# Kernel tuning notes

Hardware: AMD Instinct MI355X
Metric: run time of the kernel (lower is better)

## Reference

```python
import jax, jax.numpy as jnp
import numpy as np

B, T, D, H = 4, 2048, 1024, 16
HD = D // H

def setup_inputs() -> dict:
    key = jax.random.key(0)
    ks = jax.random.split(key, 12)
    s = 0.02
    return {
        "query": jax.random.normal(ks[0], (B, T, D), dtype=jnp.float32),
        "key_": jax.random.normal(ks[1], (B, T, D), dtype=jnp.float32),
        "value": jax.random.normal(ks[2], (B, T, D), dtype=jnp.float32),
        "attention_mask": jnp.zeros((B, T, T), dtype=bool),
        "Wq": jax.random.normal(ks[3], (D, D), dtype=jnp.float32) * s,
        "bq": jnp.zeros((D,), dtype=jnp.float32),
        "Wk": jax.random.normal(ks[4], (D, D), dtype=jnp.float32) * s,
        "bk": jnp.zeros((D,), dtype=jnp.float32),
        "Wv": jax.random.normal(ks[5], (D, D), dtype=jnp.float32) * s,
        "bv": jnp.zeros((D,), dtype=jnp.float32),
        "Wo": jax.random.normal(ks[6], (D, D), dtype=jnp.float32) * s,
        "bo": jnp.zeros((D,), dtype=jnp.float32),
    }

def reference(query, key_, value, attention_mask, Wq, bq, Wk, bk, Wv, bv, Wo, bo):
    scale = 1.0 / jnp.sqrt(jnp.float32(HD))
    # projections (torch Linear: x @ W.T + b), split heads -> [B, H, T, HD]
    q = (query @ Wq.T + bq).reshape(B, T, H, HD).transpose(0, 2, 1, 3)
    k = (key_ @ Wk.T + bk).reshape(B, T, H, HD).transpose(0, 2, 1, 3)
    v = (value @ Wv.T + bv).reshape(B, T, H, HD).transpose(0, 2, 1, 3)
    scores = jnp.einsum('bhqd,bhkd->bhqk', q, k) * scale  # [B,H,T,T]
    mask = attention_mask[:, None, :, :]  # [B,1,T,T], True = masked
    scores = jnp.where(mask, -jnp.inf, scores)
    attn = jax.nn.softmax(scores, axis=-1)
    out = jnp.einsum('bhqk,bhkd->bhqd', attn, v)  # [B,H,T,HD]
    out = out.transpose(0, 2, 1, 3).reshape(B, T, D)
    return out @ Wo.T + bo
```

## Files before the change

### kernel.cpp

```cpp
#include <hip/hip_runtime.h>
#include <hip/hip_bf16.h>
#include <math.h>


typedef short bf16x8 __attribute__((ext_vector_type(8)));
typedef short bf16x4 __attribute__((ext_vector_type(4)));
typedef float f32x4  __attribute__((ext_vector_type(4)));
typedef float f32x16 __attribute__((ext_vector_type(16)));
typedef unsigned u32x4v __attribute__((ext_vector_type(4)));

#define DEV __device__ __forceinline__

DEV short f2bf(float f) {
    union { float f; unsigned u; } x; x.f = f;
    unsigned r = x.u + 0x7fffu + ((x.u >> 16) & 1u);
    return (short)(r >> 16);
}

DEV unsigned cvtpk(float lo, float hi) {
    unsigned r;
    asm("v_cvt_pk_bf16_f32 %0, %1, %2" : "=v"(r) : "v"(lo), "v"(hi));
    return r;
}

DEV void pl32swap(unsigned &a, unsigned &b) {
    asm volatile("v_permlane32_swap_b32 %0, %1" : "+v"(a), "+v"(b));
}

DEV float fexp2(float x) {
    float r;
    asm("v_exp_f32 %0, %1\n\ts_nop 0" : "=v"(r) : "v"(x));
    return r;
}

DEV void gload16(const void* g, void* lds_wave_base) {
    __builtin_amdgcn_global_load_lds(
        (const __attribute__((address_space(1))) void*)g,
        (__attribute__((address_space(3))) void*)lds_wave_base, 16, 0, 0);
}

DEV f32x4 mfma16(bf16x8 a, bf16x8 b, f32x4 c) {
    return __builtin_amdgcn_mfma_f32_16x16x32_bf16(a, b, c, 0, 0, 0);
}
DEV f32x16 mfma32(bf16x8 a, bf16x8 b, f32x16 c) {
    return __builtin_amdgcn_mfma_f32_32x32x16_bf16(a, b, c, 0, 0, 0);
}

__global__ __launch_bounds__(256) void cvt_one(const float* __restrict__ in,
                                               short* __restrict__ out) {
    int i = (blockIdx.x * 256 + threadIdx.x) * 8;
    f32x4 a = *(const f32x4*)(in + i);
    f32x4 b = *(const f32x4*)(in + i + 4);
    bf16x8 v;
    v[0]=f2bf(a[0]); v[1]=f2bf(a[1]); v[2]=f2bf(a[2]); v[3]=f2bf(a[3]);
    v[4]=f2bf(b[0]); v[5]=f2bf(b[1]); v[6]=f2bf(b[2]); v[7]=f2bf(b[3]);
    *(bf16x8*)(out + i) = v;
}

__global__ __launch_bounds__(256) void cvt_w4(
    const float* __restrict__ a, const float* __restrict__ b,
    const float* __restrict__ c, const float* __restrict__ d,
    short* __restrict__ oa, short* __restrict__ ob,
    short* __restrict__ oc, short* __restrict__ od) {
    const int sel = blockIdx.x >> 9;
    const float* in = sel == 0 ? a : sel == 1 ? b : sel == 2 ? c : d;
    short* out      = sel == 0 ? oa : sel == 1 ? ob : sel == 2 ? oc : od;
    int i = ((blockIdx.x & 511) * 256 + threadIdx.x) * 8;
    f32x4 x = *(const f32x4*)(in + i);
    f32x4 y = *(const f32x4*)(in + i + 4);
    bf16x8 v;
    v[0]=f2bf(x[0]); v[1]=f2bf(x[1]); v[2]=f2bf(x[2]); v[3]=f2bf(x[3]);
    v[4]=f2bf(y[0]); v[5]=f2bf(y[1]); v[6]=f2bf(y[2]); v[7]=f2bf(y[3]);
    *(bf16x8*)(out + i) = v;
}

template<int EPI>
__global__ __launch_bounds__(256) void gemm_bt(
    const short* __restrict__ A, const short* __restrict__ W,
    const float* __restrict__ bias, void* __restrict__ Cp, float epiScale)
{
    __shared__ short Alds[2][4096];
    __shared__ short Blds[2][4096];

    const int t = threadIdx.x;
    const int wave = t >> 6, lane = t & 63;
    const int lr = lane & 15, lg = lane >> 4;
    const int wg = (blockIdx.x & 7) * 64 + (blockIdx.x >> 3);
    const int m0 = (wg >> 3) * 128, n0 = (wg & 7) * 128;
    const int wr = wave >> 1, wc = wave & 1;

    const int o0 = t * 16,        kb0 = o0 >> 11, row0 = (o0 >> 4) & 127;
    const int o1 = 4096 + t * 16, kb1 = o1 >> 11, row1 = (o1 >> 4) & 127;
    const short* As0 = A + (size_t)(m0 + row0) * 1024 + kb0 * 8;
    const short* As1 = A + (size_t)(m0 + row1) * 1024 + kb1 * 8;
    const short* Ws0 = W + (size_t)(n0 + row0) * 1024 + kb0 * 8;
    const short* Ws1 = W + (size_t)(n0 + row1) * 1024 + kb1 * 8;

    auto stage = [&](short* dA, short* dB, int k0) {
        gload16(As0 + k0, (char*)dA + wave * 1024);
        gload16(As1 + k0, (char*)dA + 4096 + wave * 1024);
        gload16(Ws0 + k0, (char*)dB + wave * 1024);
        gload16(Ws1 + k0, (char*)dB + 4096 + wave * 1024);
    };

    f32x4 acc[4][4] = {};

    stage(Alds[0], Blds[0], 0);

    auto kstep = [&](int ts, int BUF) {
        if (ts < 31) {
            stage(Alds[BUF ^ 1], Blds[BUF ^ 1], (ts + 1) * 32);
            asm volatile("s_waitcnt vmcnt(4)" ::: "memory");
        } else {
            asm volatile("s_waitcnt vmcnt(0)" ::: "memory");
        }
        __builtin_amdgcn_s_barrier();
        bf16x8 af[4], bfr[4];
        #pragma unroll
        for (int mi = 0; mi < 4; mi++)
            af[mi] = *(const bf16x8*)(Alds[BUF] + lg * 1024 + (wr * 64 + mi * 16 + lr) * 8);
        #pragma unroll
        for (int ni = 0; ni < 4; ni++)
            bfr[ni] = *(const bf16x8*)(Blds[BUF] + lg * 1024 + (wc * 64 + ni * 16 + lr) * 8);
        #pragma unroll
        for (int mi = 0; mi < 4; mi++)
            #pragma unroll
            for (int ni = 0; ni < 4; ni++)
                acc[mi][ni] = mfma16(af[mi], bfr[ni], acc[mi][ni]);
        __builtin_amdgcn_s_barrier();
    };

    #pragma unroll 1
    for (int it = 0; it < 16; ++it) { kstep(2 * it, 0); kstep(2 * it + 1, 1); }

    #pragma unroll
    for (int mi = 0; mi < 4; mi++) {
        #pragma unroll
        for (int ni = 0; ni < 4; ni++) {
            const int n      = n0 + wc * 64 + ni * 16 + lr;
            const int m_base = m0 + wr * 64 + mi * 16 + lg * 4;
            const float bv   = bias[n];
            f32x4 a = acc[mi][ni];
            if constexpr (EPI == 0) {
                short* C = (short*)Cp;
                #pragma unroll
                for (int r = 0; r < 4; r++)
                    C[(size_t)(m_base + r) * 1024 + n] = f2bf((a[r] + bv) * epiScale);
            } else if constexpr (EPI == 2) {
                short* C = (short*)Cp;
                const int b = m_base >> 11, tt = m_base & 2047;
                bf16x4 p;
                #pragma unroll
                for (int r = 0; r < 4; r++) p[r] = f2bf(a[r] + bv);
                *(bf16x4*)(C + (size_t)b * 2097152 + (size_t)n * 2048 + tt) = p;
            } else {
                float* C = (float*)Cp;
                #pragma unroll
                for (int r = 0; r < 4; r++)
                    C[(size_t)(m_base + r) * 1024 + n] = a[r] + bv;
            }
        }
    }
}

__global__ __launch_bounds__(256) void mask_scan(const unsigned char* __restrict__ mask,
                                                 unsigned char* __restrict__ flags) {
    __shared__ int anyk[32];
    const int t = threadIdx.x, kt = t & 31, g = t >> 5;
    const int b = blockIdx.x >> 6, qt = blockIdx.x & 63;
    if (t < 32) anyk[t] = 0;
    __syncthreads();
    unsigned acc = 0;
    const unsigned char* base = mask + ((size_t)b * 2048 + qt * 32 + g * 4) * 2048 + kt * 64;
    #pragma unroll
    for (int rr = 0; rr < 4; rr++) {
        const uint4* p = (const uint4*)(base + (size_t)rr * 2048);
        #pragma unroll
        for (int s = 0; s < 4; s++) { uint4 v = p[s]; acc |= v.x | v.y | v.z | v.w; }
    }
    if (acc) anyk[kt] = 1;
    __syncthreads();
    if (t < 32) flags[((size_t)b * 64 + qt) * 32 + t] = (unsigned char)anyk[t];
}

__global__ __launch_bounds__(256, 2) void attn_fwd2(
    const short* __restrict__ Q, const short* __restrict__ K,
    const short* __restrict__ Vt, const unsigned char* __restrict__ mask,
    const unsigned char* __restrict__ flags, short* __restrict__ O)
{
    __shared__ short lds[2][2][4096];

    const int t = threadIdx.x, wave = t >> 6, lane = t & 63;
    const int j31 = lane & 31, hi = lane >> 5;

    const int raw = blockIdx.x;
    const int wg  = (raw & 7) * 128 + (raw >> 3);
    const int qblk = wg & 15, bh = wg >> 4;
    const int h = bh & 15, b = bh >> 4;
    const int q0 = qblk * 128 + wave * 32;

    bf16x8 qf[4];
    {
        const short* qp = Q + ((size_t)b * 2048 + q0 + j31) * 1024 + h * 64 + hi * 8;
        #pragma unroll
        for (int ck = 0; ck < 4; ck++) qf[ck] = *(const bf16x8*)(qp + ck * 16);
    }
    unsigned long long fmask;
    {
        unsigned char fb = flags[((size_t)b * 64 + qblk * 4 + wave) * 32 + j31];
        fmask = __ballot(fb != 0);
    }

    const short* Kg = K + ((size_t)b * 2048) * 1024 + h * 64;
    const short* Vg = Vt + (size_t)b * 2097152 + (size_t)h * 64 * 2048;

    auto stage = [&](short* dK, short* dV, int tk) {
        #pragma unroll
        for (int i = 0; i < 2; i++) {
            const int slot = i * 256 + t, row = slot >> 3;
            const int cs = ((slot & 7) ^ (row & 7)) * 8;
            gload16(Kg + (size_t)(tk + row) * 1024 + cs, dK + i * 2048 + wave * 512);
            gload16(Vg + (size_t)row * 2048 + tk + cs, dV + i * 2048 + wave * 512);
        }
    };

    stage(&lds[0][0][0], &lds[0][1][0], 0);

    f32x16 oA = {}, oB = {};
    float m = -1e30f, l = 0.f;
    const int sw = j31 & 7;

    auto tile = [&](int J, int BUF) {
        if (J < 31) {
            stage(&lds[BUF ^ 1][0][0], &lds[BUF ^ 1][1][0], (J + 1) * 64);
            asm volatile("s_waitcnt vmcnt(4)" ::: "memory");
        } else {
            asm volatile("s_waitcnt vmcnt(0)" ::: "memory");
        }
        __builtin_amdgcn_s_barrier();
        const short* ldsK = &lds[BUF][0][0];
        const short* ldsV = &lds[BUF][1][0];

        f32x16 sA = {}, sB = {};
        __builtin_amdgcn_s_setprio(1);
        #pragma unroll
        for (int ck = 0; ck < 4; ck++) {
            bf16x8 kf0 = *(const bf16x8*)(ldsK + j31 * 64        + (((2*ck + hi) ^ sw) * 8));
            bf16x8 kf1 = *(const bf16x8*)(ldsK + (32 + j31) * 64 + (((2*ck + hi) ^ sw) * 8));
            sA = mfma32(kf0, qf[ck], sA);
            sB = mfma32(kf1, qf[ck], sB);
        }
        __builtin_amdgcn_s_setprio(0);

        if ((fmask >> J) & 1ULL) {
            const unsigned char* mp = mask + ((size_t)b * 2048 + q0 + j31) * 2048
                                           + (size_t)J * 64 + hi * 4;
            #pragma unroll
            for (int a2 = 0; a2 < 2; a2++)
                #pragma unroll
                for (int rg = 0; rg < 4; rg++) {
                    unsigned mb = *(const unsigned*)(mp + a2 * 32 + rg * 8);
                    #pragma unroll
                    for (int e = 0; e < 4; e++) {
                        if ((mb >> (8 * e)) & 0xFFu) {
                            if (a2 == 0) sA[rg * 4 + e] = -1e30f;
                            else         sB[rg * 4 + e] = -1e30f;
                        }
                    }
                }
        }

        float tm = fmaxf(sA[0], sA[1]);
        #pragma unroll
        for (int r = 2; r < 16; r += 2) tm = fmaxf(fmaxf(tm, sA[r]), sA[r + 1]);
        #pragma unroll
        for (int r = 0; r < 16; r += 2) tm = fmaxf(fmaxf(tm, sB[r]), sB[r + 1]);
        tm = fmaxf(tm, __shfl_xor(tm, 32));
        if (!__all(tm <= m + 8.f)) {
            const float mnew = fmaxf(m, tm);
            const float fs = fexp2(m - mnew);
            m = mnew; l *= fs;
            #pragma unroll
            for (int r = 0; r < 16; r++) { oA[r] *= fs; oB[r] *= fs; }
        }
        float ps = 0.f;
        #pragma unroll
        for (int r = 0; r < 16; r++) { sA[r] = fexp2(sA[r] - m); ps += sA[r]; }
        #pragma unroll
        for (int r = 0; r < 16; r++) { sB[r] = fexp2(sB[r] - m); ps += sB[r]; }
        ps += __shfl_xor(ps, 32);
        l += ps;

        bf16x8 pb[4];
        #pragma unroll
        for (int c = 0; c < 4; c++) {
            const int rb = 8 * (c & 1);
            unsigned A0, B0, A1, B1;
            if (c < 2) {
                A0 = cvtpk(sA[rb],     sA[rb + 1]); B0 = cvtpk(sA[rb + 4], sA[rb + 5]);
                A1 = cvtpk(sA[rb + 2], sA[rb + 3]); B1 = cvtpk(sA[rb + 6], sA[rb + 7]);
            } else {
                A0 = cvtpk(sB[rb],     sB[rb + 1]); B0 = cvtpk(sB[rb + 4], sB[rb + 5]);
                A1 = cvtpk(sB[rb + 2], sB[rb + 3]); B1 = cvtpk(sB[rb + 6], sB[rb + 7]);
            }
            pl32swap(A0, B0); pl32swap(A1, B1);
            union { unsigned u[4]; bf16x8 v; } pu;
            pu.u[0] = A0; pu.u[1] = A1; pu.u[2] = B0; pu.u[3] = B1;
            pb[c] = pu.v;
        }

        __builtin_amdgcn_s_setprio(1);
        #pragma unroll
        for (int c = 0; c < 4; c++) {
            bf16x8 vf0 = *(const bf16x8*)(ldsV + j31 * 64        + (((2*c + hi) ^ sw) * 8));
            bf16x8 vf1 = *(const bf16x8*)(ldsV + (32 + j31) * 64 + (((2*c + hi) ^ sw) * 8));
            oA = mfma32(vf0, pb[c], oA);
            oB = mfma32(vf1, pb[c], oB);
        }
        __builtin_amdgcn_s_setprio(0);
        __builtin_amdgcn_s_barrier();
    };

    #pragma unroll 1
    for (int jj = 0; jj < 16; ++jj) { tile(2 * jj, 0); tile(2 * jj + 1, 1); }

    __syncthreads();
    unsigned* ow = (unsigned*)&lds[0][0][0] + wave * (32 * 34);
    const float inv = 1.f / l;
    #pragma unroll
    for (int o = 0; o < 2; o++)
        #pragma unroll
        for (int rp = 0; rp < 8; rp++) {
            const int r  = 2 * rp;
            const int hd = 2 * (rp & 1) + 8 * (rp >> 1) + 4 * hi + 32 * o;
            const float v0 = (o ? oB[r]     : oA[r])     * inv;
            const float v1 = (o ? oB[r + 1] : oA[r + 1]) * inv;
            ow[j31 * 34 + (hd >> 1)] = cvtpk(v0, v1);
        }
    __syncthreads();
    {
        const size_t orow = ((size_t)b * 2048 + q0 + j31) * 1024 + h * 64 + hi * 32;
        unsigned* gout = (unsigned*)(O + orow);
        const unsigned* src = ow + j31 * 34 + hi * 16;
        #pragma unroll
        for (int i = 0; i < 4; i++) {
            u32x4v v;
            v[0] = src[i*4]; v[1] = src[i*4+1]; v[2] = src[i*4+2]; v[3] = src[i*4+3];
            *(u32x4v*)(gout + i * 4) = v;
        }
    }
}

extern "C" void kernel_launch(void* const* d_in, const int* in_sizes, int n_in,
                              void* d_out, int out_size, void* d_ws, size_t ws_size,
                              hipStream_t stream)
{
    const float* query = (const float*)d_in[0];
    const float* key_  = (const float*)d_in[1];
    const float* value = (const float*)d_in[2];
    const unsigned char* amask = (const unsigned char*)d_in[3];
    const float* Wq = (const float*)d_in[4];
    const float* bq = (const float*)d_in[5];
    const float* Wk = (const float*)d_in[6];
    const float* bk = (const float*)d_in[7];
    const float* Wv = (const float*)d_in[8];
    const float* bv = (const float*)d_in[9];
    const float* Wo = (const float*)d_in[10];
    const float* bo = (const float*)d_in[11];
    float* out = (float*)d_out;

    char* ws = (char*)d_ws;
    const size_t MB = 1024 * 1024;
    short* Wqb = (short*)(ws + 0 * MB);
    short* Wkb = (short*)(ws + 2 * MB);
    short* Wvb = (short*)(ws + 4 * MB);
    short* Wob = (short*)(ws + 6 * MB);
    short* Qb  = (short*)(ws + 8 * MB);
    short* Kb  = (short*)(ws + 24 * MB);
    short* Vtb = (short*)(ws + 40 * MB);
    short* Xb  = (short*)(ws + 56 * MB);
    unsigned char* flagsb = (unsigned char*)(ws + 0 * MB);

    cvt_w4<<<2048, 256, 0, stream>>>(Wq, Wk, Wv, Wo, Wqb, Wkb, Wvb, Wob);

    const float qscale = 0.125f * 1.44269504088896f;
    cvt_one<<<4096, 256, 0, stream>>>(query, Xb);
    gemm_bt<0><<<512, 256, 0, stream>>>(Xb, Wqb, bq, Qb, qscale);
    cvt_one<<<4096, 256, 0, stream>>>(key_, Xb);
    gemm_bt<0><<<512, 256, 0, stream>>>(Xb, Wkb, bk, Kb, 1.0f);
    cvt_one<<<4096, 256, 0, stream>>>(value, Xb);
    gemm_bt<2><<<512, 256, 0, stream>>>(Xb, Wvb, bv, Vtb, 1.0f);

    mask_scan<<<256, 256, 0, stream>>>(amask, flagsb);

    attn_fwd2<<<1024, 256, 0, stream>>>(Qb, Kb, Vtb, amask, flagsb, Xb);

    gemm_bt<3><<<512, 256, 0, stream>>>(Xb, Wob, bo, out, 1.0f);
}
```

Measured before the change: 286.1 us.

## Fuse fp32 input conversion into batched QKV GEMM and widen attention KV tiles

Drops the three separate activation-conversion kernels and the three projection GEMM launches. A single gemm_qkv kernel now loads fp32 activations into registers, converts them to bf16 into LDS, and prefetches the next k-step. The attention kernel processes 128-key tiles instead of 64, using a larger LDS buffer and a wider V swizzle. It also computes the softmax row sum with an extra MFMA against a ones vector rather than scalar adds plus a shuffle. The weight conversion switches to packed cvt instructions. The aim is to cut launches and intermediate bf16 traffic and to halve the attention barrier count, at the cost of more register pressure and LDS use per block.

```diff
diff --git a/kernel.cpp b/kernel.cpp
--- a/kernel.cpp
+++ b/kernel.cpp
@@ -44,17 +44,6 @@
 }
 DEV f32x16 mfma32(bf16x8 a, bf16x8 b, f32x16 c) {
     return __builtin_amdgcn_mfma_f32_32x32x16_bf16(a, b, c, 0, 0, 0);
-}
-
-__global__ __launch_bounds__(256) void cvt_one(const float* __restrict__ in,
-                                               short* __restrict__ out) {
-    int i = (blockIdx.x * 256 + threadIdx.x) * 8;
-    f32x4 a = *(const f32x4*)(in + i);
-    f32x4 b = *(const f32x4*)(in + i + 4);
-    bf16x8 v;
-    v[0]=f2bf(a[0]); v[1]=f2bf(a[1]); v[2]=f2bf(a[2]); v[3]=f2bf(a[3]);
-    v[4]=f2bf(b[0]); v[5]=f2bf(b[1]); v[6]=f2bf(b[2]); v[7]=f2bf(b[3]);
-    *(bf16x8*)(out + i) = v;
 }
 
 __global__ __launch_bounds__(256) void cvt_w4(
@@ -68,16 +57,124 @@
     int i = ((blockIdx.x & 511) * 256 + threadIdx.x) * 8;
     f32x4 x = *(const f32x4*)(in + i);
     f32x4 y = *(const f32x4*)(in + i + 4);
-    bf16x8 v;
-    v[0]=f2bf(x[0]); v[1]=f2bf(x[1]); v[2]=f2bf(x[2]); v[3]=f2bf(x[3]);
-    v[4]=f2bf(y[0]); v[5]=f2bf(y[1]); v[6]=f2bf(y[2]); v[7]=f2bf(y[3]);
-    *(bf16x8*)(out + i) = v;
-}
-
-template<int EPI>
-__global__ __launch_bounds__(256) void gemm_bt(
+    union { unsigned u[4]; bf16x8 v; } p;
+    p.u[0] = cvtpk(x[0], x[1]); p.u[1] = cvtpk(x[2], x[3]);
+    p.u[2] = cvtpk(y[0], y[1]); p.u[3] = cvtpk(y[2], y[3]);
+    *(bf16x8*)(out + i) = p.v;
+}
+
+__global__ __launch_bounds__(256) void gemm_qkv(
+    const float* __restrict__ Aq, const float* __restrict__ Ak, const float* __restrict__ Av,
+    const short* __restrict__ Wqb, const short* __restrict__ Wkb, const short* __restrict__ Wvb,
+    const float* __restrict__ bqp, const float* __restrict__ bkp, const float* __restrict__ bvp,
+    short* __restrict__ Qo, short* __restrict__ Ko, short* __restrict__ Vo, float qscale)
+{
+    __shared__ short Alds[2][4096];
+    __shared__ short Blds[2][4096];
+
+    const int t = threadIdx.x, wave = t >> 6, lane = t & 63;
+    const int lr = lane & 15, lg = lane >> 4;
+    const int raw = blockIdx.x;
+    const int wg = (raw & 7) * 192 + (raw >> 3);
+    const int sel = wg >> 9, inner = wg & 511;
+    const int m0 = (inner >> 3) * 128, n0 = (inner & 7) * 128;
+    const int wr = wave >> 1, wc = wave & 1;
+
+    const float* A    = sel == 0 ? Aq  : sel == 1 ? Ak  : Av;
+    const short* W    = sel == 0 ? Wqb : sel == 1 ? Wkb : Wvb;
+    const float* bias = sel == 0 ? bqp : sel == 1 ? bkp : bvp;
+
+    const int arow = t & 127, kh = t >> 7;
+    const float* Asrc = A + (size_t)(m0 + arow) * 1024 + kh * 16;
+    const int o0 = t * 16,        kb0 = o0 >> 11, row0 = (o0 >> 4) & 127;
+    const int o1 = 4096 + t * 16, kb1 = o1 >> 11, row1 = (o1 >> 4) & 127;
+    const short* Ws0 = W + (size_t)(n0 + row0) * 1024 + kb0 * 8;
+    const short* Ws1 = W + (size_t)(n0 + row1) * 1024 + kb1 * 8;
+
+    f32x4 ar0, ar1, ar2, ar3;
+    auto aload = [&](int k0) {
+        ar0 = *(const f32x4*)(Asrc + k0);
+        ar1 = *(const f32x4*)(Asrc + k0 + 4);
+        ar2 = *(const f32x4*)(Asrc + k0 + 8);
+        ar3 = *(const f32x4*)(Asrc + k0 + 12);
+    };
+    auto awrite = [&](short* dst0) {
+        union { unsigned u[4]; bf16x8 v; } p0, p1;
+        p0.u[0] = cvtpk(ar0[0], ar0[1]); p0.u[1] = cvtpk(ar0[2], ar0[3]);
+        p0.u[2] = cvtpk(ar1[0], ar1[1]); p0.u[3] = cvtpk(ar1[2], ar1[3]);
+        p1.u[0] = cvtpk(ar2[0], ar2[1]); p1.u[1] = cvtpk(ar2[2], ar2[3]);
+        p1.u[2] = cvtpk(ar3[0], ar3[1]); p1.u[3] = cvtpk(ar3[2], ar3[3]);
+        short* dst = dst0 + (kh * 2) * 1024 + arow * 8;
+        *(bf16x8*)dst          = p0.v;
+        *(bf16x8*)(dst + 1024) = p1.v;
+    };
+    auto wstage = [&](short* dB, int k0) {
+        gload16(Ws0 + k0, (char*)dB + wave * 1024);
+        gload16(Ws1 + k0, (char*)dB + 4096 + wave * 1024);
+    };
+
+    f32x4 acc[4][4] = {};
+
+    aload(0);
+    asm volatile("s_waitcnt vmcnt(0)" ::: "memory");
+    awrite(Alds[0]);
+    wstage(Blds[0], 0);
+    aload(32);
+
+    #pragma unroll 1
+    for (int ts = 0; ts < 32; ++ts) {
+        const int B = ts & 1;
+        if (ts < 31) asm volatile("s_waitcnt vmcnt(4) lgkmcnt(0)" ::: "memory");
+        else         asm volatile("s_waitcnt vmcnt(0) lgkmcnt(0)" ::: "memory");
+        __builtin_amdgcn_s_barrier();
+        bf16x8 af[4], bfr[4];
+        #pragma unroll
+        for (int mi = 0; mi < 4; mi++)
+            af[mi] = *(const bf16x8*)(Alds[B] + lg * 1024 + (wr * 64 + mi * 16 + lr) * 8);
+        #pragma unroll
+        for (int ni = 0; ni < 4; ni++)
+            bfr[ni] = *(const bf16x8*)(Blds[B] + lg * 1024 + (wc * 64 + ni * 16 + lr) * 8);
+        if (ts < 31) wstage(Blds[B ^ 1], (ts + 1) * 32);
+        #pragma unroll
+        for (int mi = 0; mi < 4; mi++)
+            #pragma unroll
+            for (int ni = 0; ni < 4; ni++)
+                acc[mi][ni] = mfma16(af[mi], bfr[ni], acc[mi][ni]);
+        if (ts < 31) {
+            asm volatile("s_waitcnt vmcnt(2)" ::: "memory");
+            awrite(Alds[B ^ 1]);
+            if (ts < 30) aload((ts + 2) * 32);
+        }
+    }
+
+    #pragma unroll
+    for (int mi = 0; mi < 4; mi++) {
+        #pragma unroll
+        for (int ni = 0; ni < 4; ni++) {
+            const int n      = n0 + wc * 64 + ni * 16 + lr;
+            const int m_base = m0 + wr * 64 + mi * 16 + lg * 4;
+            const float bv   = bias[n];
+            f32x4 a = acc[mi][ni];
+            if (sel == 2) {
+                const int bb = m_base >> 11, tt = m_base & 2047;
+                bf16x4 p;
+                #pragma unroll
+                for (int r = 0; r < 4; r++) p[r] = f2bf(a[r] + bv);
+                *(bf16x4*)(Vo + (size_t)bb * 2097152 + (size_t)n * 2048 + tt) = p;
+            } else {
+                short* C = sel ? Ko : Qo;
+                const float sc = sel ? 1.0f : qscale;
+                #pragma unroll
+                for (int r = 0; r < 4; r++)
+                    C[(size_t)(m_base + r) * 1024 + n] = f2bf((a[r] + bv) * sc);
+            }
+        }
+    }
+}
+
+__global__ __launch_bounds__(256) void gemm_out(
     const short* __restrict__ A, const short* __restrict__ W,
-    const float* __restrict__ bias, void* __restrict__ Cp, float epiScale)
+    const float* __restrict__ bias, float* __restrict__ C)
 {
     __shared__ short Alds[2][4096];
     __shared__ short Blds[2][4096];
@@ -104,7 +201,6 @@
     };
 
     f32x4 acc[4][4] = {};
-
     stage(Alds[0], Blds[0], 0);
 
     auto kstep = [&](int ts, int BUF) {
@@ -141,24 +237,9 @@
             const int m_base = m0 + wr * 64 + mi * 16 + lg * 4;
             const float bv   = bias[n];
             f32x4 a = acc[mi][ni];
-            if constexpr (EPI == 0) {
-                short* C = (short*)Cp;
-                #pragma unroll
-                for (int r = 0; r < 4; r++)
-                    C[(size_t)(m_base + r) * 1024 + n] = f2bf((a[r] + bv) * epiScale);
-            } else if constexpr (EPI == 2) {
-                short* C = (short*)Cp;
-                const int b = m_base >> 11, tt = m_base & 2047;
-                bf16x4 p;
-                #pragma unroll
-                for (int r = 0; r < 4; r++) p[r] = f2bf(a[r] + bv);
-                *(bf16x4*)(C + (size_t)b * 2097152 + (size_t)n * 2048 + tt) = p;
-            } else {
-                float* C = (float*)Cp;
-                #pragma unroll
-                for (int r = 0; r < 4; r++)
-                    C[(size_t)(m_base + r) * 1024 + n] = a[r] + bv;
-            }
+            #pragma unroll
+            for (int r = 0; r < 4; r++)
+                C[(size_t)(m_base + r) * 1024 + n] = a[r] + bv;
         }
     }
 }
@@ -183,12 +264,12 @@
     if (t < 32) flags[((size_t)b * 64 + qt) * 32 + t] = (unsigned char)anyk[t];
 }
 
-__global__ __launch_bounds__(256, 2) void attn_fwd2(
+__global__ __launch_bounds__(256, 2) void attn_fwd3(
     const short* __restrict__ Q, const short* __restrict__ K,
     const short* __restrict__ Vt, const unsigned char* __restrict__ mask,
     const unsigned char* __restrict__ flags, short* __restrict__ O)
 {
-    __shared__ short lds[2][2][4096];
+    __shared__ short lds[2][2][8192];
 
     const int t = threadIdx.x, wave = t >> 6, lane = t & 63;
     const int j31 = lane & 31, hi = lane >> 5;
@@ -210,30 +291,34 @@
         unsigned char fb = flags[((size_t)b * 64 + qblk * 4 + wave) * 32 + j31];
         fmask = __ballot(fb != 0);
     }
+    bf16x8 onesv;
+    #pragma unroll
+    for (int i = 0; i < 8; i++) onesv[i] = (short)0x3F80;
 
     const short* Kg = K + ((size_t)b * 2048) * 1024 + h * 64;
     const short* Vg = Vt + (size_t)b * 2097152 + (size_t)h * 64 * 2048;
 
     auto stage = [&](short* dK, short* dV, int tk) {
         #pragma unroll
-        for (int i = 0; i < 2; i++) {
-            const int slot = i * 256 + t, row = slot >> 3;
-            const int cs = ((slot & 7) ^ (row & 7)) * 8;
-            gload16(Kg + (size_t)(tk + row) * 1024 + cs, dK + i * 2048 + wave * 512);
-            gload16(Vg + (size_t)row * 2048 + tk + cs, dV + i * 2048 + wave * 512);
+        for (int i = 0; i < 4; i++) {
+            const int s = i * 256 + t;
+            const int rK = s >> 3, cK = ((s & 7) ^ (rK & 7)) * 8;
+            gload16(Kg + (size_t)(tk + rK) * 1024 + cK, dK + i * 2048 + wave * 512);
+            const int rV = s >> 4, cV = ((s & 15) ^ (rV & 15)) * 8;
+            gload16(Vg + (size_t)rV * 2048 + tk + cV, dV + i * 2048 + wave * 512);
         }
     };
 
     stage(&lds[0][0][0], &lds[0][1][0], 0);
 
-    f32x16 oA = {}, oB = {};
-    float m = -1e30f, l = 0.f;
-    const int sw = j31 & 7;
+    f32x16 oA = {}, oB = {}, accL = {};
+    float m = -1e30f;
+    const int swk = j31 & 7, swv = j31 & 15;
 
     auto tile = [&](int J, int BUF) {
-        if (J < 31) {
-            stage(&lds[BUF ^ 1][0][0], &lds[BUF ^ 1][1][0], (J + 1) * 64);
-            asm volatile("s_waitcnt vmcnt(4)" ::: "memory");
+        if (J < 15) {
+            stage(&lds[BUF ^ 1][0][0], &lds[BUF ^ 1][1][0], (J + 1) * 128);
+            asm volatile("s_waitcnt vmcnt(8)" ::: "memory");
         } else {
             asm volatile("s_waitcnt vmcnt(0)" ::: "memory");
         }
@@ -241,33 +326,35 @@
         const short* ldsK = &lds[BUF][0][0];
         const short* ldsV = &lds[BUF][1][0];
 
-        f32x16 sA = {}, sB = {};
+        f32x16 sA = {}, sB = {}, sC = {}, sD = {};
         __builtin_amdgcn_s_setprio(1);
         #pragma unroll
         for (int ck = 0; ck < 4; ck++) {
-            bf16x8 kf0 = *(const bf16x8*)(ldsK + j31 * 64        + (((2*ck + hi) ^ sw) * 8));
-            bf16x8 kf1 = *(const bf16x8*)(ldsK + (32 + j31) * 64 + (((2*ck + hi) ^ sw) * 8));
-            sA = mfma32(kf0, qf[ck], sA);
-            sB = mfma32(kf1, qf[ck], sB);
+            const int co = ((2 * ck + hi) ^ swk) * 8;
+            bf16x8 k0 = *(const bf16x8*)(ldsK + (j31      ) * 64 + co);
+            bf16x8 k1 = *(const bf16x8*)(ldsK + (32 + j31) * 64 + co);
+            bf16x8 k2 = *(const bf16x8*)(ldsK + (64 + j31) * 64 + co);
+            bf16x8 k3 = *(const bf16x8*)(ldsK + (96 + j31) * 64 + co);
+            sA = mfma32(k0, qf[ck], sA);
+            sB = mfma32(k1, qf[ck], sB);
+            sC = mfma32(k2, qf[ck], sC);
+            sD = mfma32(k3, qf[ck], sD);
         }
         __builtin_amdgcn_s_setprio(0);
 
-        if ((fmask >> J) & 1ULL) {
+        if ((fmask >> (2 * J)) & 3ULL) {
             const unsigned char* mp = mask + ((size_t)b * 2048 + q0 + j31) * 2048
-                                           + (size_t)J * 64 + hi * 4;
-            #pragma unroll
-            for (int a2 = 0; a2 < 2; a2++)
+                                           + (size_t)J * 128 + hi * 4;
+            auto apply = [&](f32x16& sX, int X) {
                 #pragma unroll
                 for (int rg = 0; rg < 4; rg++) {
-                    unsigned mb = *(const unsigned*)(mp + a2 * 32 + rg * 8);
+                    unsigned mb = *(const unsigned*)(mp + X * 32 + rg * 8);
                     #pragma unroll
-                    for (int e = 0; e < 4; e++) {
-                        if ((mb >> (8 * e)) & 0xFFu) {
-                            if (a2 == 0) sA[rg * 4 + e] = -1e30f;
-                            else         sB[rg * 4 + e] = -1e30f;
-                        }
-                    }
+                    for (int e = 0; e < 4; e++)
+                        if ((mb >> (8 * e)) & 0xFFu) sX[rg * 4 + e] = -1e30f;
                 }
+            };
+            apply(sA, 0); apply(sB, 1); apply(sC, 2); apply(sD, 3);
         }
 
         float tm = fmaxf(sA[0], sA[1]);
@@ -275,58 +362,55 @@
         for (int r = 2; r < 16; r += 2) tm = fmaxf(fmaxf(tm, sA[r]), sA[r + 1]);
         #pragma unroll
         for (int r = 0; r < 16; r += 2) tm = fmaxf(fmaxf(tm, sB[r]), sB[r + 1]);
+        #pragma unroll
+        for (int r = 0; r < 16; r += 2) tm = fmaxf(fmaxf(tm, sC[r]), sC[r + 1]);
+        #pragma unroll
+        for (int r = 0; r < 16; r += 2) tm = fmaxf(fmaxf(tm, sD[r]), sD[r + 1]);
         tm = fmaxf(tm, __shfl_xor(tm, 32));
         if (!__all(tm <= m + 8.f)) {
             const float mnew = fmaxf(m, tm);
             const float fs = fexp2(m - mnew);
-            m = mnew; l *= fs;
+            m = mnew;
             #pragma unroll
             for (int r = 0; r < 16; r++) { oA[r] *= fs; oB[r] *= fs; }
-        }
-        float ps = 0.f;
-        #pragma unroll
-        for (int r = 0; r < 16; r++) { sA[r] = fexp2(sA[r] - m); ps += sA[r]; }
-        #pragma unroll
-        for (int r = 0; r < 16; r++) { sB[r] = fexp2(sB[r] - m); ps += sB[r]; }
-        ps += __shfl_xor(ps, 32);
-        l += ps;
-
-        bf16x8 pb[4];
-        #pragma unroll
-        for (int c = 0; c < 4; c++) {
+            accL[0] *= fs;
+        }
+        #pragma unroll
+        for (int r = 0; r < 16; r++) sA[r] = fexp2(sA[r] - m);
+        #pragma unroll
+        for (int r = 0; r < 16; r++) sB[r] = fexp2(sB[r] - m);
+        #pragma unroll
+        for (int r = 0; r < 16; r++) sC[r] = fexp2(sC[r] - m);
+        #pragma unroll
+        for (int r = 0; r < 16; r++) sD[r] = fexp2(sD[r] - m);
+
+        __builtin_amdgcn_s_setprio(1);
+        #pragma unroll
+        for (int c = 0; c < 8; c++) {
+            const f32x16& sX = (c < 2) ? sA : (c < 4) ? sB : (c < 6) ? sC : sD;
             const int rb = 8 * (c & 1);
-            unsigned A0, B0, A1, B1;
-            if (c < 2) {
-                A0 = cvtpk(sA[rb],     sA[rb + 1]); B0 = cvtpk(sA[rb + 4], sA[rb + 5]);
-                A1 = cvtpk(sA[rb + 2], sA[rb + 3]); B1 = cvtpk(sA[rb + 6], sA[rb + 7]);
-            } else {
-                A0 = cvtpk(sB[rb],     sB[rb + 1]); B0 = cvtpk(sB[rb + 4], sB[rb + 5]);
-                A1 = cvtpk(sB[rb + 2], sB[rb + 3]); B1 = cvtpk(sB[rb + 6], sB[rb + 7]);
-            }
+            unsigned A0 = cvtpk(sX[rb],     sX[rb + 1]), B0 = cvtpk(sX[rb + 4], sX[rb + 5]);
+            unsigned A1 = cvtpk(sX[rb + 2], sX[rb + 3]), B1 = cvtpk(sX[rb + 6], sX[rb + 7]);
             pl32swap(A0, B0); pl32swap(A1, B1);
             union { unsigned u[4]; bf16x8 v; } pu;
             pu.u[0] = A0; pu.u[1] = A1; pu.u[2] = B0; pu.u[3] = B1;
-            pb[c] = pu.v;
-        }
-
-        __builtin_amdgcn_s_setprio(1);
-        #pragma unroll
-        for (int c = 0; c < 4; c++) {
-            bf16x8 vf0 = *(const bf16x8*)(ldsV + j31 * 64        + (((2*c + hi) ^ sw) * 8));
-            bf16x8 vf1 = *(const bf16x8*)(ldsV + (32 + j31) * 64 + (((2*c + hi) ^ sw) * 8));
-            oA = mfma32(vf0, pb[c], oA);
-            oB = mfma32(vf1, pb[c], oB);
+            const int co = ((2 * c + hi) ^ swv) * 8;
+            bf16x8 v0 = *(const bf16x8*)(ldsV + (j31      ) * 128 + co);
+            bf16x8 v1 = *(const bf16x8*)(ldsV + (32 + j31) * 128 + co);
+            oA   = mfma32(v0, pu.v, oA);
+            oB   = mfma32(v1, pu.v, oB);
+            accL = mfma32(onesv, pu.v, accL);
         }
         __builtin_amdgcn_s_setprio(0);
         __builtin_amdgcn_s_barrier();
     };
 
     #pragma unroll 1
-    for (int jj = 0; jj < 16; ++jj) { tile(2 * jj, 0); tile(2 * jj + 1, 1); }
+    for (int jj = 0; jj < 8; ++jj) { tile(2 * jj, 0); tile(2 * jj + 1, 1); }
 
     __syncthreads();
     unsigned* ow = (unsigned*)&lds[0][0][0] + wave * (32 * 34);
-    const float inv = 1.f / l;
+    const float inv = 1.f / accL[0];
     #pragma unroll
     for (int o = 0; o < 2; o++)
         #pragma unroll
@@ -384,16 +468,12 @@
     cvt_w4<<<2048, 256, 0, stream>>>(Wq, Wk, Wv, Wo, Wqb, Wkb, Wvb, Wob);
 
     const float qscale = 0.125f * 1.44269504088896f;
-    cvt_one<<<4096, 256, 0, stream>>>(query, Xb);
-    gemm_bt<0><<<512, 256, 0, stream>>>(Xb, Wqb, bq, Qb, qscale);
-    cvt_one<<<4096, 256, 0, stream>>>(key_, Xb);
-    gemm_bt<0><<<512, 256, 0, stream>>>(Xb, Wkb, bk, Kb, 1.0f);
-    cvt_one<<<4096, 256, 0, stream>>>(value, Xb);
-    gemm_bt<2><<<512, 256, 0, stream>>>(Xb, Wvb, bv, Vtb, 1.0f);
+    gemm_qkv<<<1536, 256, 0, stream>>>(query, key_, value, Wqb, Wkb, Wvb,
+                                       bq, bk, bv, Qb, Kb, Vtb, qscale);
 
     mask_scan<<<256, 256, 0, stream>>>(amask, flagsb);
 
-    attn_fwd2<<<1024, 256, 0, stream>>>(Qb, Kb, Vtb, amask, flagsb, Xb);
-
-    gemm_bt<3><<<512, 256, 0, stream>>>(Xb, Wob, bo, out, 1.0f);
-}
+    attn_fwd3<<<1024, 256, 0, stream>>>(Qb, Kb, Vtb, amask, flagsb, Xb);
+
+    gemm_out<<<512, 256, 0, stream>>>(Xb, Wob, bo, out);
+}
```

Result: no change. 289.6 us (+1.2%).
